# Kernel optimization log

Measured on AMD Instinct MI355X. Metric: run time of the kernel, lower is better.

The kernel has to match this reference:

```python
import jax, jax.numpy as jnp
import numpy as np

B, DIN, DOUT, NW = 32768, 768, 768, 48
NH = NW // 3  # num_haar == num_mexican == num_morlet == 16 for NW=48
OMEGA0 = 5.0
LN_EPS = 1e-5


def setup_inputs() -> dict:
    key = jax.random.key(0)
    ks = jax.random.split(key, 6)
    x = jax.random.normal(ks[0], (B, DIN), dtype=jnp.float32)
    # kaiming-normal-ish fan_in init for linear layers, zero bias
    W = jax.random.normal(ks[1], (DOUT, DIN), dtype=jnp.float32) / np.sqrt(DIN)
    b = jnp.zeros((DOUT,), jnp.float32)
    Wp = jax.random.normal(ks[2], (NW, DIN), dtype=jnp.float32) / np.sqrt(DIN)
    bp = jnp.zeros((NW,), jnp.float32)
    Wc = jax.random.normal(ks[3], (DOUT, NW), dtype=jnp.float32) / np.sqrt(NW)
    bc = jnp.zeros((DOUT,), jnp.float32)
    # mixed-type init: per-family logspace scales / linspace translations
    scales = jnp.asarray(np.concatenate([
        np.logspace(-0.5, 0.5, NH),
        np.logspace(-0.3, 0.7, NH),
        np.logspace(-0.3, 0.7, NW - 2 * NH)]), jnp.float32)
    translations = jnp.asarray(np.concatenate([
        np.linspace(-1.5, 1.5, NH),
        np.linspace(-1.5, 1.5, NH),
        np.linspace(-1.5, 1.5, NW - 2 * NH)]), jnp.float32)
    gamma = jnp.ones((DOUT,), jnp.float32)
    beta = jnp.zeros((DOUT,), jnp.float32)
    return {"x": x, "W": W, "b": b, "Wp": Wp, "bp": bp, "Wc": Wc,
            "bc": bc, "scales": scales, "translations": translations,
            "gamma": gamma, "beta": beta}


def _wavelet_basis(s):
    # s: [B, NW] already scaled/translated; columns split by family
    dt = s.dtype
    sh = s[:, :NH]
    haar = (((sh >= 0) & (sh < 0.5)).astype(dt)
            - ((sh >= 0.5) & (sh < 1.0)).astype(dt))
    sm = s[:, NH:2 * NH]
    mexican = (1.0 - sm * sm) * jnp.exp(-0.5 * sm * sm)
    so = s[:, 2 * NH:]
    morlet = jnp.cos(OMEGA0 * so) * jnp.exp(-0.5 * so * so)
    return jnp.concatenate([haar, mexican, morlet], axis=1)


def reference(x, W, b, Wp, bp, Wc, bc, scales, translations, gamma, beta):
    direct = x @ W.T + b                              # [B, DOUT]
    wi = x @ Wp.T + bp                                # [B, NW]
    s = (wi - translations) / scales                  # [B, NW]
    wav = jax.nn.gelu(_wavelet_basis(s), approximate=False)
    wpath = wav @ Wc.T + bc                           # [B, DOUT]
    h = direct + wpath
    mu = jnp.mean(h, axis=-1, keepdims=True)
    var = jnp.mean((h - mu) ** 2, axis=-1, keepdims=True)
    return (h - mu) * jax.lax.rsqrt(var + LN_EPS) * gamma + beta
```

## Files before the change

kernel.cpp:

```cpp
#include <hip/hip_runtime.h>
#include <math.h>


#define B_SZ  32768
#define DIN   768
#define DOUT  768
#define NWAV  48

#define WF_OFF   0
#define WPH_OFF  589824
#define WPL_OFF  638976
#define WCF_OFF  688128

typedef short bf16x8 __attribute__((ext_vector_type(8)));
typedef float f32x16 __attribute__((ext_vector_type(16)));

__device__ __forceinline__ float bf2f(short u) {
    union { unsigned int i; float f; } v;
    v.i = ((unsigned int)(unsigned short)u) << 16;
    return v.f;
}
__device__ __forceinline__ short f2bf(float f) {
    union { float f; unsigned int i; } v; v.f = f;
    unsigned int r = v.i + 0x7FFFu + ((v.i >> 16) & 1u);
    return (short)(r >> 16);
}

__global__ __launch_bounds__(256) void pack_kernel(
    const float* __restrict__ W, const float* __restrict__ Wp,
    const float* __restrict__ Wc, short* __restrict__ ws)
{
    const int gw = (blockIdx.x * 256 + threadIdx.x) >> 6;
    const int L  = threadIdx.x & 63;
    const int lm = L & 31, half = L >> 5;

    if (gw < 1152) {
        const int cb = gw / 48, kb = gw % 48;
        const int row = cb * 32 + lm;
        const int k = kb * 16 + half * 8;
        bf16x8 o;
#pragma unroll
        for (int j = 0; j < 8; j++) o[j] = f2bf(W[(size_t)row * DIN + k + j]);
        *reinterpret_cast<bf16x8*>(&ws[WF_OFF + (size_t)gw * 512 + L * 8]) = o;
    } else if (gw < 1248) {
        const int t = gw - 1152;
        const int ct = t / 48, kb = t % 48;
        const int j = ct * 32 + lm;
        const int k = kb * 16 + half * 8;
        bf16x8 h, l;
#pragma unroll
        for (int jj = 0; jj < 8; jj++) {
            float v = (j < NWAV) ? Wp[(size_t)j * DIN + k + jj] : 0.f;
            const short hh = f2bf(v);
            h[jj] = hh;
            l[jj] = f2bf(v - bf2f(hh));
        }
        *reinterpret_cast<bf16x8*>(&ws[WPH_OFF + (size_t)t * 512 + L * 8]) = h;
        *reinterpret_cast<bf16x8*>(&ws[WPL_OFF + (size_t)t * 512 + L * 8]) = l;
    } else if (gw < 1320) {
        const int t = gw - 1248;
        const int cb = t / 3, kb = t % 3;
        const int row = cb * 32 + lm;
        const int k = kb * 16 + half * 8;
        bf16x8 o;
#pragma unroll
        for (int jj = 0; jj < 8; jj++) o[jj] = f2bf(Wc[(size_t)row * NWAV + k + jj]);
        *reinterpret_cast<bf16x8*>(&ws[WCF_OFF + (size_t)t * 512 + L * 8]) = o;
    }
}

__global__ __launch_bounds__(512, 2) void fused_kernel(
    const float* __restrict__ x, const short* __restrict__ ws,
    const float* __restrict__ Wp,
    const float* __restrict__ bp, const float* __restrict__ sc,
    const float* __restrict__ tr,
    const float* __restrict__ bb, const float* __restrict__ bc,
    const float* __restrict__ gm, const float* __restrict__ bt,
    float* __restrict__ out)
{
    __shared__ __align__(16) short xh[2][64 * 72];
    __shared__ __align__(16) short xl[2][64 * 72];
    __shared__ float redS[64 * 8], redQ[64 * 8];
    __shared__ float muA[64], rsA[64];
    __shared__ unsigned flags[64];
    __shared__ double dred[8];

    const short* WF  = ws + WF_OFF;
    const short* WPH = ws + WPH_OFF;
    const short* WPL = ws + WPL_OFF;
    const short* WCF = ws + WCF_OFF;

    const int tid = threadIdx.x;
    const int r0  = blockIdx.x * 64;
    const int L   = tid & 63;
    const int wv  = __builtin_amdgcn_readfirstlane(tid >> 6);
    const int lm  = L & 31, half = L >> 5;
    const int L8  = L * 8;
    const bool wi = (wv < 4);
    const int wv3 = wv * 3;
    const int wrt = wv & 1, wct = wv >> 1;
    const int wct48 = wct * 48;

    if (tid < 64) flags[tid] = 0u;

    f32x16 acc[2][3];
#pragma unroll
    for (int rt = 0; rt < 2; rt++)
#pragma unroll
        for (int ct = 0; ct < 3; ct++)
#pragma unroll
            for (int g = 0; g < 16; g++) acc[rt][ct][g] = 0.f;
    f32x16 wacc;
#pragma unroll
    for (int g = 0; g < 16; g++) wacc[g] = 0.f;

    const int srow = tid >> 3;
    const int sk   = (tid & 7) * 8;

    {
        const float4* xp = reinterpret_cast<const float4*>(&x[(size_t)(r0 + srow) * DIN + sk]);
        const float4 v0 = xp[0], v1 = xp[1];
        const float f[8] = {v0.x, v0.y, v0.z, v0.w, v1.x, v1.y, v1.z, v1.w};
        bf16x8 hh, ll;
#pragma unroll
        for (int i = 0; i < 8; i++) {
            const short h = f2bf(f[i]);
            hh[i] = h;
            ll[i] = f2bf(f[i] - bf2f(h));
        }
        *reinterpret_cast<bf16x8*>(&xh[0][srow * 72 + sk]) = hh;
        *reinterpret_cast<bf16x8*>(&xl[0][srow * 72 + sk]) = ll;
    }
    __syncthreads();

    for (int k0i = 0; k0i < 12; ++k0i) {
        const int cur = k0i & 1;
        const int kb0 = k0i * 4;

        bf16x8 bfr[4][3];
#pragma unroll
        for (int ks = 0; ks < 4; ++ks)
#pragma unroll
            for (int ct = 0; ct < 3; ++ct)
                bfr[ks][ct] = *reinterpret_cast<const bf16x8*>(
                    &WF[((size_t)((wv3 + ct) * 48 + kb0 + ks)) * 512 + L8]);
        bf16x8 bwh[4], bwl[4];
        if (wi) {
#pragma unroll
            for (int ks = 0; ks < 4; ++ks) {
                bwh[ks] = *reinterpret_cast<const bf16x8*>(
                    &WPH[((size_t)(wct48 + kb0 + ks)) * 512 + L8]);
                bwl[ks] = *reinterpret_cast<const bf16x8*>(
                    &WPL[((size_t)(wct48 + kb0 + ks)) * 512 + L8]);
            }
        }

        float4 v0, v1;
        if (k0i < 11) {
            const float4* xp = reinterpret_cast<const float4*>(
                &x[(size_t)(r0 + srow) * DIN + (k0i + 1) * 64 + sk]);
            v0 = xp[0]; v1 = xp[1];
        }

        __builtin_amdgcn_sched_barrier(0);

#pragma unroll
        for (int ks = 0; ks < 4; ++ks) {
            const bf16x8 a0 = *reinterpret_cast<bf16x8*>(
                &xh[cur][lm * 72 + ks * 16 + half * 8]);
            const bf16x8 a1 = *reinterpret_cast<bf16x8*>(
                &xh[cur][(32 + lm) * 72 + ks * 16 + half * 8]);
#pragma unroll
            for (int ct = 0; ct < 3; ++ct) {
                acc[0][ct] = __builtin_amdgcn_mfma_f32_32x32x16_bf16(a0, bfr[ks][ct], acc[0][ct], 0, 0, 0);
                acc[1][ct] = __builtin_amdgcn_mfma_f32_32x32x16_bf16(a1, bfr[ks][ct], acc[1][ct], 0, 0, 0);
            }
            if (wi) {
                const bf16x8 ah = wrt ? a1 : a0;
                const bf16x8 al = *reinterpret_cast<bf16x8*>(
                    &xl[cur][(wrt * 32 + lm) * 72 + ks * 16 + half * 8]);
                wacc = __builtin_amdgcn_mfma_f32_32x32x16_bf16(ah, bwl[ks], wacc, 0, 0, 0);
                wacc = __builtin_amdgcn_mfma_f32_32x32x16_bf16(al, bwh[ks], wacc, 0, 0, 0);
                wacc = __builtin_amdgcn_mfma_f32_32x32x16_bf16(ah, bwh[ks], wacc, 0, 0, 0);
            }
        }

        if (k0i < 11) {
            const float f[8] = {v0.x, v0.y, v0.z, v0.w, v1.x, v1.y, v1.z, v1.w};
            bf16x8 hh, ll;
#pragma unroll
            for (int i = 0; i < 8; i++) {
                const short h = f2bf(f[i]);
                hh[i] = h;
                ll[i] = f2bf(f[i] - bf2f(h));
            }
            *reinterpret_cast<bf16x8*>(&xh[1 - cur][srow * 72 + sk]) = hh;
            *reinterpret_cast<bf16x8*>(&xl[1 - cur][srow * 72 + sk]) = ll;
        }
        __syncthreads();
    }

    short* wavL = &xh[0][0];
    if (wi) {
        const int j = wct * 32 + lm;
        if (j < NWAV) {
            const float bpv = bp[j], scv = sc[j], trv = tr[j];
#pragma unroll
            for (int g = 0; g < 16; ++g) {
                const int rowl = wrt * 32 + (g & 3) + 8 * (g >> 2) + 4 * half;
                const float wiv = wacc[g] + bpv;
                const float s = (wiv - trv) / scv;
                float w;
                if (j < 16) {
                    const float dmin = fminf(fabsf(s), fminf(fabsf(s - 0.5f), fabsf(s - 1.0f)));
                    if (dmin < 2e-4f) atomicOr(&flags[rowl], 1u << j);
                    w = (s >= 0.f && s < 0.5f) ? 1.f : ((s >= 0.5f && s < 1.f) ? -1.f : 0.f);
                } else if (j < 32) {
                    w = (1.f - s * s) * expf(-0.5f * s * s);
                } else {
                    w = cosf(5.f * s) * expf(-0.5f * s * s);
                }
                const float gel = 0.5f * w * (1.f + erff(w * 0.70710678118654752f));
                wavL[rowl * 72 + j] = f2bf(gel);
            }
        }
    }
    __syncthreads();

#pragma unroll 1
    for (int fr = 0; fr < 64; ++fr) {
        unsigned m = flags[fr];
        while (m) {
            const int j = __ffs(m) - 1;
            m &= m - 1;
            const float* xr = &x[(size_t)(r0 + fr) * DIN];
            const float* wr = &Wp[(size_t)j * DIN];
            double a = (double)xr[tid] * (double)wr[tid];
            if (tid < DIN - 512)
                a += (double)xr[tid + 512] * (double)wr[tid + 512];
            a += __shfl_xor(a, 1);  a += __shfl_xor(a, 2);
            a += __shfl_xor(a, 4);  a += __shfl_xor(a, 8);
            a += __shfl_xor(a, 16); a += __shfl_xor(a, 32);
            if (L == 0) dred[wv] = a;
            __syncthreads();
            if (tid == 0) {
                double wid = (double)bp[j];
#pragma unroll
                for (int i = 0; i < 8; i++) wid += dred[i];
                const double sd = (wid - (double)tr[j]) / (double)sc[j];
                const double w = (sd >= 0.0 && sd < 0.5) ? 1.0
                               : ((sd >= 0.5 && sd < 1.0) ? -1.0 : 0.0);
                const double gel = 0.5 * w * (1.0 + erf(w * 0.70710678118654752));
                wavL[fr * 72 + j] = f2bf((float)gel);
            }
            __syncthreads();
        }
    }

#pragma unroll
    for (int ks = 0; ks < 3; ++ks) {
        const bf16x8 a0 = *reinterpret_cast<bf16x8*>(&wavL[lm * 72 + ks * 16 + half * 8]);
        const bf16x8 a1 = *reinterpret_cast<bf16x8*>(&wavL[(32 + lm) * 72 + ks * 16 + half * 8]);
#pragma unroll
        for (int ct = 0; ct < 3; ++ct) {
            const bf16x8 b = *reinterpret_cast<const bf16x8*>(
                &WCF[((size_t)((wv3 + ct) * 3 + ks)) * 512 + L8]);
            acc[0][ct] = __builtin_amdgcn_mfma_f32_32x32x16_bf16(a0, b, acc[0][ct], 0, 0, 0);
            acc[1][ct] = __builtin_amdgcn_mfma_f32_32x32x16_bf16(a1, b, acc[1][ct], 0, 0, 0);
        }
    }

    float bias[3], gmv[3], btv[3];
#pragma unroll
    for (int ct = 0; ct < 3; ++ct) {
        const int col = wv * 96 + ct * 32 + lm;
        bias[ct] = bb[col] + bc[col];
        gmv[ct] = gm[col];
        btv[ct] = bt[col];
    }
#pragma unroll
    for (int rt = 0; rt < 2; ++rt) {
#pragma unroll
        for (int g = 0; g < 16; ++g) {
            const float v0 = acc[rt][0][g] + bias[0];
            const float v1 = acc[rt][1][g] + bias[1];
            const float v2 = acc[rt][2][g] + bias[2];
            acc[rt][0][g] = v0; acc[rt][1][g] = v1; acc[rt][2][g] = v2;
            float s1 = v0 + v1 + v2;
            float s2 = v0 * v0 + v1 * v1 + v2 * v2;
            s1 += __shfl_xor(s1, 1);  s2 += __shfl_xor(s2, 1);
            s1 += __shfl_xor(s1, 2);  s2 += __shfl_xor(s2, 2);
            s1 += __shfl_xor(s1, 4);  s2 += __shfl_xor(s2, 4);
            s1 += __shfl_xor(s1, 8);  s2 += __shfl_xor(s2, 8);
            s1 += __shfl_xor(s1, 16); s2 += __shfl_xor(s2, 16);
            if (lm == 0) {
                const int rowl = rt * 32 + (g & 3) + 8 * (g >> 2) + 4 * half;
                redS[rowl * 8 + wv] = s1;
                redQ[rowl * 8 + wv] = s2;
            }
        }
    }
    __syncthreads();
    if (tid < 64) {
        float S = 0.f, Q = 0.f;
#pragma unroll
        for (int i = 0; i < 8; i++) { S += redS[tid * 8 + i]; Q += redQ[tid * 8 + i]; }
        const float mu = S * (1.f / 768.f);
        const float var = Q * (1.f / 768.f) - mu * mu;
        muA[tid] = mu;
        rsA[tid] = rsqrtf(var + 1e-5f);
    }
    __syncthreads();

#pragma unroll
    for (int rt = 0; rt < 2; ++rt) {
#pragma unroll
        for (int g = 0; g < 16; ++g) {
            const int rowl = rt * 32 + (g & 3) + 8 * (g >> 2) + 4 * half;
            const float mu = muA[rowl], rs = rsA[rowl];
            float* orow = &out[(size_t)(r0 + rowl) * DOUT + wv * 96 + lm];
#pragma unroll
            for (int ct = 0; ct < 3; ++ct) {
                orow[ct * 32] = (acc[rt][ct][g] - mu) * rs * gmv[ct] + btv[ct];
            }
        }
    }
}

extern "C" void kernel_launch(void* const* d_in, const int* in_sizes, int n_in,
                              void* d_out, int out_size, void* d_ws, size_t ws_size,
                              hipStream_t stream)
{
    const float* x  = (const float*)d_in[0];
    const float* W  = (const float*)d_in[1];
    const float* b  = (const float*)d_in[2];
    const float* Wp = (const float*)d_in[3];
    const float* bp = (const float*)d_in[4];
    const float* Wc = (const float*)d_in[5];
    const float* bc = (const float*)d_in[6];
    const float* sc = (const float*)d_in[7];
    const float* tr = (const float*)d_in[8];
    const float* gm = (const float*)d_in[9];
    const float* bt = (const float*)d_in[10];
    float* out = (float*)d_out;
    short* ws  = (short*)d_ws;

    pack_kernel<<<dim3(330), dim3(256), 0, stream>>>(W, Wp, Wc, ws);
    fused_kernel<<<dim3(B_SZ / 64), dim3(512), 0, stream>>>(
        x, ws, Wp, bp, sc, tr, b, bc, gm, bt, out);
}
```

Measured before the change: 264.9 us.

## Merge weight packing into a persistent cooperative kernel with grid sync and float4 stores

```diff
diff --git a/kernel.cpp b/kernel.cpp
--- a/kernel.cpp
+++ b/kernel.cpp
@@ -1,5 +1,8 @@
 #include <hip/hip_runtime.h>
+#include <hip/hip_cooperative_groups.h>
 #include <math.h>
+
+namespace cg = cooperative_groups;
 
 
 #define B_SZ  32768
@@ -26,52 +29,10 @@
     return (short)(r >> 16);
 }
 
-__global__ __launch_bounds__(256) void pack_kernel(
-    const float* __restrict__ W, const float* __restrict__ Wp,
-    const float* __restrict__ Wc, short* __restrict__ ws)
-{
-    const int gw = (blockIdx.x * 256 + threadIdx.x) >> 6;
-    const int L  = threadIdx.x & 63;
-    const int lm = L & 31, half = L >> 5;
-
-    if (gw < 1152) {
-        const int cb = gw / 48, kb = gw % 48;
-        const int row = cb * 32 + lm;
-        const int k = kb * 16 + half * 8;
-        bf16x8 o;
-#pragma unroll
-        for (int j = 0; j < 8; j++) o[j] = f2bf(W[(size_t)row * DIN + k + j]);
-        *reinterpret_cast<bf16x8*>(&ws[WF_OFF + (size_t)gw * 512 + L * 8]) = o;
-    } else if (gw < 1248) {
-        const int t = gw - 1152;
-        const int ct = t / 48, kb = t % 48;
-        const int j = ct * 32 + lm;
-        const int k = kb * 16 + half * 8;
-        bf16x8 h, l;
-#pragma unroll
-        for (int jj = 0; jj < 8; jj++) {
-            float v = (j < NWAV) ? Wp[(size_t)j * DIN + k + jj] : 0.f;
-            const short hh = f2bf(v);
-            h[jj] = hh;
-            l[jj] = f2bf(v - bf2f(hh));
-        }
-        *reinterpret_cast<bf16x8*>(&ws[WPH_OFF + (size_t)t * 512 + L * 8]) = h;
-        *reinterpret_cast<bf16x8*>(&ws[WPL_OFF + (size_t)t * 512 + L * 8]) = l;
-    } else if (gw < 1320) {
-        const int t = gw - 1248;
-        const int cb = t / 3, kb = t % 3;
-        const int row = cb * 32 + lm;
-        const int k = kb * 16 + half * 8;
-        bf16x8 o;
-#pragma unroll
-        for (int jj = 0; jj < 8; jj++) o[jj] = f2bf(Wc[(size_t)row * NWAV + k + jj]);
-        *reinterpret_cast<bf16x8*>(&ws[WCF_OFF + (size_t)t * 512 + L * 8]) = o;
-    }
-}
-
 __global__ __launch_bounds__(512, 2) void fused_kernel(
-    const float* __restrict__ x, const short* __restrict__ ws,
-    const float* __restrict__ Wp,
+    const float* __restrict__ x,  const float* __restrict__ W,
+    const float* __restrict__ Wp, const float* __restrict__ Wc,
+    short* __restrict__ ws,
     const float* __restrict__ bp, const float* __restrict__ sc,
     const float* __restrict__ tr,
     const float* __restrict__ bb, const float* __restrict__ bc,
@@ -85,13 +46,7 @@
     __shared__ unsigned flags[64];
     __shared__ double dred[8];
 
-    const short* WF  = ws + WF_OFF;
-    const short* WPH = ws + WPH_OFF;
-    const short* WPL = ws + WPL_OFF;
-    const short* WCF = ws + WCF_OFF;
-
     const int tid = threadIdx.x;
-    const int r0  = blockIdx.x * 64;
     const int L   = tid & 63;
     const int wv  = __builtin_amdgcn_readfirstlane(tid >> 6);
     const int lm  = L & 31, half = L >> 5;
@@ -101,91 +56,74 @@
     const int wrt = wv & 1, wct = wv >> 1;
     const int wct48 = wct * 48;
 
-    if (tid < 64) flags[tid] = 0u;
-
-    f32x16 acc[2][3];
-#pragma unroll
-    for (int rt = 0; rt < 2; rt++)
-#pragma unroll
-        for (int ct = 0; ct < 3; ct++)
-#pragma unroll
-            for (int g = 0; g < 16; g++) acc[rt][ct][g] = 0.f;
-    f32x16 wacc;
-#pragma unroll
-    for (int g = 0; g < 16; g++) wacc[g] = 0.f;
+    {
+        const int gw = blockIdx.x * 8 + wv;
+        if (gw < 1152) {
+            const int cb = gw / 48, kb = gw % 48;
+            const int row = cb * 32 + lm;
+            const int k = kb * 16 + half * 8;
+            bf16x8 o;
+#pragma unroll
+            for (int j = 0; j < 8; j++) o[j] = f2bf(W[(size_t)row * DIN + k + j]);
+            *reinterpret_cast<bf16x8*>(&ws[WF_OFF + (size_t)gw * 512 + L8]) = o;
+        } else if (gw < 1248) {
+            const int t = gw - 1152;
+            const int ct = t / 48, kb = t % 48;
+            const int j = ct * 32 + lm;
+            const int k = kb * 16 + half * 8;
+            bf16x8 h, l;
+#pragma unroll
+            for (int jj = 0; jj < 8; jj++) {
+                float v = (j < NWAV) ? Wp[(size_t)j * DIN + k + jj] : 0.f;
+                const short hh = f2bf(v);
+                h[jj] = hh;
+                l[jj] = f2bf(v - bf2f(hh));
+            }
+            *reinterpret_cast<bf16x8*>(&ws[WPH_OFF + (size_t)t * 512 + L8]) = h;
+            *reinterpret_cast<bf16x8*>(&ws[WPL_OFF + (size_t)t * 512 + L8]) = l;
+        } else if (gw < 1320) {
+            const int t = gw - 1248;
+            const int cb = t / 3, kb = t % 3;
+            const int row = cb * 32 + lm;
+            const int k = kb * 16 + half * 8;
+            bf16x8 o;
+#pragma unroll
+            for (int jj = 0; jj < 8; jj++) o[jj] = f2bf(Wc[(size_t)row * NWAV + k + jj]);
+            *reinterpret_cast<bf16x8*>(&ws[WCF_OFF + (size_t)t * 512 + L8]) = o;
+        }
+    }
+    cg::this_grid().sync();
+
+    const short* WF  = ws + WF_OFF;
+    const short* WPH = ws + WPH_OFF;
+    const short* WPL = ws + WPL_OFF;
+    const short* WCF = ws + WCF_OFF;
 
     const int srow = tid >> 3;
     const int sk   = (tid & 7) * 8;
 
-    {
-        const float4* xp = reinterpret_cast<const float4*>(&x[(size_t)(r0 + srow) * DIN + sk]);
-        const float4 v0 = xp[0], v1 = xp[1];
-        const float f[8] = {v0.x, v0.y, v0.z, v0.w, v1.x, v1.y, v1.z, v1.w};
-        bf16x8 hh, ll;
-#pragma unroll
-        for (int i = 0; i < 8; i++) {
-            const short h = f2bf(f[i]);
-            hh[i] = h;
-            ll[i] = f2bf(f[i] - bf2f(h));
-        }
-        *reinterpret_cast<bf16x8*>(&xh[0][srow * 72 + sk]) = hh;
-        *reinterpret_cast<bf16x8*>(&xl[0][srow * 72 + sk]) = ll;
-    }
-    __syncthreads();
-
-    for (int k0i = 0; k0i < 12; ++k0i) {
-        const int cur = k0i & 1;
-        const int kb0 = k0i * 4;
-
-        bf16x8 bfr[4][3];
-#pragma unroll
-        for (int ks = 0; ks < 4; ++ks)
-#pragma unroll
-            for (int ct = 0; ct < 3; ++ct)
-                bfr[ks][ct] = *reinterpret_cast<const bf16x8*>(
-                    &WF[((size_t)((wv3 + ct) * 48 + kb0 + ks)) * 512 + L8]);
-        bf16x8 bwh[4], bwl[4];
-        if (wi) {
-#pragma unroll
-            for (int ks = 0; ks < 4; ++ks) {
-                bwh[ks] = *reinterpret_cast<const bf16x8*>(
-                    &WPH[((size_t)(wct48 + kb0 + ks)) * 512 + L8]);
-                bwl[ks] = *reinterpret_cast<const bf16x8*>(
-                    &WPL[((size_t)(wct48 + kb0 + ks)) * 512 + L8]);
-            }
-        }
-
-        float4 v0, v1;
-        if (k0i < 11) {
-            const float4* xp = reinterpret_cast<const float4*>(
-                &x[(size_t)(r0 + srow) * DIN + (k0i + 1) * 64 + sk]);
-            v0 = xp[0]; v1 = xp[1];
-        }
-
-        __builtin_amdgcn_sched_barrier(0);
-
-#pragma unroll
-        for (int ks = 0; ks < 4; ++ks) {
-            const bf16x8 a0 = *reinterpret_cast<bf16x8*>(
-                &xh[cur][lm * 72 + ks * 16 + half * 8]);
-            const bf16x8 a1 = *reinterpret_cast<bf16x8*>(
-                &xh[cur][(32 + lm) * 72 + ks * 16 + half * 8]);
-#pragma unroll
-            for (int ct = 0; ct < 3; ++ct) {
-                acc[0][ct] = __builtin_amdgcn_mfma_f32_32x32x16_bf16(a0, bfr[ks][ct], acc[0][ct], 0, 0, 0);
-                acc[1][ct] = __builtin_amdgcn_mfma_f32_32x32x16_bf16(a1, bfr[ks][ct], acc[1][ct], 0, 0, 0);
-            }
-            if (wi) {
-                const bf16x8 ah = wrt ? a1 : a0;
-                const bf16x8 al = *reinterpret_cast<bf16x8*>(
-                    &xl[cur][(wrt * 32 + lm) * 72 + ks * 16 + half * 8]);
-                wacc = __builtin_amdgcn_mfma_f32_32x32x16_bf16(ah, bwl[ks], wacc, 0, 0, 0);
-                wacc = __builtin_amdgcn_mfma_f32_32x32x16_bf16(al, bwh[ks], wacc, 0, 0, 0);
-                wacc = __builtin_amdgcn_mfma_f32_32x32x16_bf16(ah, bwh[ks], wacc, 0, 0, 0);
-            }
-        }
-
-        if (k0i < 11) {
+    const bool ib0 = (lm & 1) != 0, ib1 = (lm & 2) != 0;
+
+#pragma unroll 1
+    for (int pass = 0; pass < 2; ++pass) {
+        const int r0 = (blockIdx.x + (pass << 8)) * 64;
+
+        if (tid < 64) flags[tid] = 0u;
+
+        f32x16 acc[2][3];
+#pragma unroll
+        for (int rt = 0; rt < 2; rt++)
+#pragma unroll
+            for (int ct = 0; ct < 3; ct++)
+#pragma unroll
+                for (int g = 0; g < 16; g++) acc[rt][ct][g] = 0.f;
+        f32x16 wacc;
+#pragma unroll
+        for (int g = 0; g < 16; g++) wacc[g] = 0.f;
+
+        {
+            const float4* xp = reinterpret_cast<const float4*>(&x[(size_t)(r0 + srow) * DIN + sk]);
+            const float4 v0 = xp[0], v1 = xp[1];
             const float f[8] = {v0.x, v0.y, v0.z, v0.w, v1.x, v1.y, v1.z, v1.w};
             bf16x8 hh, ll;
 #pragma unroll
@@ -194,134 +132,231 @@
                 hh[i] = h;
                 ll[i] = f2bf(f[i] - bf2f(h));
             }
-            *reinterpret_cast<bf16x8*>(&xh[1 - cur][srow * 72 + sk]) = hh;
-            *reinterpret_cast<bf16x8*>(&xl[1 - cur][srow * 72 + sk]) = ll;
+            *reinterpret_cast<bf16x8*>(&xh[0][srow * 72 + sk]) = hh;
+            *reinterpret_cast<bf16x8*>(&xl[0][srow * 72 + sk]) = ll;
         }
         __syncthreads();
-    }
-
-    short* wavL = &xh[0][0];
-    if (wi) {
-        const int j = wct * 32 + lm;
-        if (j < NWAV) {
-            const float bpv = bp[j], scv = sc[j], trv = tr[j];
+
+        for (int k0i = 0; k0i < 12; ++k0i) {
+            const int cur = k0i & 1;
+            const int kb0 = k0i * 4;
+
+            bf16x8 bfr[4][3];
+#pragma unroll
+            for (int ks = 0; ks < 4; ++ks)
+#pragma unroll
+                for (int ct = 0; ct < 3; ++ct)
+                    bfr[ks][ct] = *reinterpret_cast<const bf16x8*>(
+                        &WF[((size_t)((wv3 + ct) * 48 + kb0 + ks)) * 512 + L8]);
+            bf16x8 bwh[4], bwl[4];
+            if (wi) {
+#pragma unroll
+                for (int ks = 0; ks < 4; ++ks) {
+                    bwh[ks] = *reinterpret_cast<const bf16x8*>(
+                        &WPH[((size_t)(wct48 + kb0 + ks)) * 512 + L8]);
+                    bwl[ks] = *reinterpret_cast<const bf16x8*>(
+                        &WPL[((size_t)(wct48 + kb0 + ks)) * 512 + L8]);
+                }
+            }
+
+            float4 v0, v1;
+            if (k0i < 11) {
+                const float4* xp = reinterpret_cast<const float4*>(
+                    &x[(size_t)(r0 + srow) * DIN + (k0i + 1) * 64 + sk]);
+                v0 = xp[0]; v1 = xp[1];
+            }
+
+            __builtin_amdgcn_sched_barrier(0);
+
+#pragma unroll
+            for (int ks = 0; ks < 4; ++ks) {
+                const bf16x8 a0 = *reinterpret_cast<bf16x8*>(
+                    &xh[cur][lm * 72 + ks * 16 + half * 8]);
+                const bf16x8 a1 = *reinterpret_cast<bf16x8*>(
+                    &xh[cur][(32 + lm) * 72 + ks * 16 + half * 8]);
+#pragma unroll
+                for (int ct = 0; ct < 3; ++ct) {
+                    acc[0][ct] = __builtin_amdgcn_mfma_f32_32x32x16_bf16(a0, bfr[ks][ct], acc[0][ct], 0, 0, 0);
+                    acc[1][ct] = __builtin_amdgcn_mfma_f32_32x32x16_bf16(a1, bfr[ks][ct], acc[1][ct], 0, 0, 0);
+                }
+                if (wi) {
+                    const bf16x8 ah = wrt ? a1 : a0;
+                    const bf16x8 al = *reinterpret_cast<bf16x8*>(
+                        &xl[cur][(wrt * 32 + lm) * 72 + ks * 16 + half * 8]);
+                    wacc = __builtin_amdgcn_mfma_f32_32x32x16_bf16(ah, bwl[ks], wacc, 0, 0, 0);
+                    wacc = __builtin_amdgcn_mfma_f32_32x32x16_bf16(al, bwh[ks], wacc, 0, 0, 0);
+                    wacc = __builtin_amdgcn_mfma_f32_32x32x16_bf16(ah, bwh[ks], wacc, 0, 0, 0);
+                }
+            }
+
+            if (k0i < 11) {
+                const float f[8] = {v0.x, v0.y, v0.z, v0.w, v1.x, v1.y, v1.z, v1.w};
+                bf16x8 hh, ll;
+#pragma unroll
+                for (int i = 0; i < 8; i++) {
+                    const short h = f2bf(f[i]);
+                    hh[i] = h;
+                    ll[i] = f2bf(f[i] - bf2f(h));
+                }
+                *reinterpret_cast<bf16x8*>(&xh[1 - cur][srow * 72 + sk]) = hh;
+                *reinterpret_cast<bf16x8*>(&xl[1 - cur][srow * 72 + sk]) = ll;
+            }
+            __syncthreads();
+        }
+
+        short* wavL = &xh[0][0];
+        if (wi) {
+            const int j = wct * 32 + lm;
+            if (j < NWAV) {
+                const float bpv = bp[j], scv = sc[j], trv = tr[j];
+#pragma unroll
+                for (int g = 0; g < 16; ++g) {
+                    const int rowl = wrt * 32 + (g & 3) + 8 * (g >> 2) + 4 * half;
+                    const float wiv = wacc[g] + bpv;
+                    const float s = (wiv - trv) / scv;
+                    float w;
+                    if (j < 16) {
+                        const float dmin = fminf(fabsf(s), fminf(fabsf(s - 0.5f), fabsf(s - 1.0f)));
+                        if (dmin < 2e-4f) atomicOr(&flags[rowl], 1u << j);
+                        w = (s >= 0.f && s < 0.5f) ? 1.f : ((s >= 0.5f && s < 1.f) ? -1.f : 0.f);
+                    } else if (j < 32) {
+                        w = (1.f - s * s) * expf(-0.5f * s * s);
+                    } else {
+                        w = cosf(5.f * s) * expf(-0.5f * s * s);
+                    }
+                    const float gel = 0.5f * w * (1.f + erff(w * 0.70710678118654752f));
+                    wavL[rowl * 72 + j] = f2bf(gel);
+                }
+            }
+        }
+        __syncthreads();
+
+#pragma unroll 1
+        for (int fr = 0; fr < 64; ++fr) {
+            unsigned m = flags[fr];
+            while (m) {
+                const int j = __ffs(m) - 1;
+                m &= m - 1;
+                const float* xr = &x[(size_t)(r0 + fr) * DIN];
+                const float* wr = &Wp[(size_t)j * DIN];
+                double a = (double)xr[tid] * (double)wr[tid];
+                if (tid < DIN - 512)
+                    a += (double)xr[tid + 512] * (double)wr[tid + 512];
+                a += __shfl_xor(a, 1);  a += __shfl_xor(a, 2);
+                a += __shfl_xor(a, 4);  a += __shfl_xor(a, 8);
+                a += __shfl_xor(a, 16); a += __shfl_xor(a, 32);
+                if (L == 0) dred[wv] = a;
+                __syncthreads();
+                if (tid == 0) {
+                    double wid = (double)bp[j];
+#pragma unroll
+                    for (int i = 0; i < 8; i++) wid += dred[i];
+                    const double sd = (wid - (double)tr[j]) / (double)sc[j];
+                    const double w = (sd >= 0.0 && sd < 0.5) ? 1.0
+                                   : ((sd >= 0.5 && sd < 1.0) ? -1.0 : 0.0);
+                    const double gel = 0.5 * w * (1.0 + erf(w * 0.70710678118654752));
+                    wavL[fr * 72 + j] = f2bf((float)gel);
+                }
+                __syncthreads();
+            }
+        }
+
+#pragma unroll
+        for (int ks = 0; ks < 3; ++ks) {
+            const bf16x8 a0 = *reinterpret_cast<bf16x8*>(&wavL[lm * 72 + ks * 16 + half * 8]);
+            const bf16x8 a1 = *reinterpret_cast<bf16x8*>(&wavL[(32 + lm) * 72 + ks * 16 + half * 8]);
+#pragma unroll
+            for (int ct = 0; ct < 3; ++ct) {
+                const bf16x8 b = *reinterpret_cast<const bf16x8*>(
+                    &WCF[((size_t)((wv3 + ct) * 3 + ks)) * 512 + L8]);
+                acc[0][ct] = __builtin_amdgcn_mfma_f32_32x32x16_bf16(a0, b, acc[0][ct], 0, 0, 0);
+                acc[1][ct] = __builtin_amdgcn_mfma_f32_32x32x16_bf16(a1, b, acc[1][ct], 0, 0, 0);
+            }
+        }
+
+        float bias[3];
+#pragma unroll
+        for (int ct = 0; ct < 3; ++ct) {
+            const int col = wv * 96 + ct * 32 + lm;
+            bias[ct] = bb[col] + bc[col];
+        }
+#pragma unroll
+        for (int rt = 0; rt < 2; ++rt) {
 #pragma unroll
             for (int g = 0; g < 16; ++g) {
-                const int rowl = wrt * 32 + (g & 3) + 8 * (g >> 2) + 4 * half;
-                const float wiv = wacc[g] + bpv;
-                const float s = (wiv - trv) / scv;
-                float w;
-                if (j < 16) {
-                    const float dmin = fminf(fabsf(s), fminf(fabsf(s - 0.5f), fabsf(s - 1.0f)));
-                    if (dmin < 2e-4f) atomicOr(&flags[rowl], 1u << j);
-                    w = (s >= 0.f && s < 0.5f) ? 1.f : ((s >= 0.5f && s < 1.f) ? -1.f : 0.f);
-                } else if (j < 32) {
-                    w = (1.f - s * s) * expf(-0.5f * s * s);
-                } else {
-                    w = cosf(5.f * s) * expf(-0.5f * s * s);
-                }
-                const float gel = 0.5f * w * (1.f + erff(w * 0.70710678118654752f));
-                wavL[rowl * 72 + j] = f2bf(gel);
-            }
-        }
-    }
-    __syncthreads();
-
-#pragma unroll 1
-    for (int fr = 0; fr < 64; ++fr) {
-        unsigned m = flags[fr];
-        while (m) {
-            const int j = __ffs(m) - 1;
-            m &= m - 1;
-            const float* xr = &x[(size_t)(r0 + fr) * DIN];
-            const float* wr = &Wp[(size_t)j * DIN];
-            double a = (double)xr[tid] * (double)wr[tid];
-            if (tid < DIN - 512)
-                a += (double)xr[tid + 512] * (double)wr[tid + 512];
-            a += __shfl_xor(a, 1);  a += __shfl_xor(a, 2);
-            a += __shfl_xor(a, 4);  a += __shfl_xor(a, 8);
-            a += __shfl_xor(a, 16); a += __shfl_xor(a, 32);
-            if (L == 0) dred[wv] = a;
-            __syncthreads();
-            if (tid == 0) {
-                double wid = (double)bp[j];
-#pragma unroll
-                for (int i = 0; i < 8; i++) wid += dred[i];
-                const double sd = (wid - (double)tr[j]) / (double)sc[j];
-                const double w = (sd >= 0.0 && sd < 0.5) ? 1.0
-                               : ((sd >= 0.5 && sd < 1.0) ? -1.0 : 0.0);
-                const double gel = 0.5 * w * (1.0 + erf(w * 0.70710678118654752));
-                wavL[fr * 72 + j] = f2bf((float)gel);
-            }
-            __syncthreads();
-        }
-    }
-
-#pragma unroll
-    for (int ks = 0; ks < 3; ++ks) {
-        const bf16x8 a0 = *reinterpret_cast<bf16x8*>(&wavL[lm * 72 + ks * 16 + half * 8]);
-        const bf16x8 a1 = *reinterpret_cast<bf16x8*>(&wavL[(32 + lm) * 72 + ks * 16 + half * 8]);
+                const float v0 = acc[rt][0][g] + bias[0];
+                const float v1 = acc[rt][1][g] + bias[1];
+                const float v2 = acc[rt][2][g] + bias[2];
+                acc[rt][0][g] = v0; acc[rt][1][g] = v1; acc[rt][2][g] = v2;
+                float s1 = v0 + v1 + v2;
+                float s2 = v0 * v0 + v1 * v1 + v2 * v2;
+                s1 += __shfl_xor(s1, 1);  s2 += __shfl_xor(s2, 1);
+                s1 += __shfl_xor(s1, 2);  s2 += __shfl_xor(s2, 2);
+                s1 += __shfl_xor(s1, 4);  s2 += __shfl_xor(s2, 4);
+                s1 += __shfl_xor(s1, 8);  s2 += __shfl_xor(s2, 8);
+                s1 += __shfl_xor(s1, 16); s2 += __shfl_xor(s2, 16);
+                if (lm == 0) {
+                    const int rowl = rt * 32 + (g & 3) + 8 * (g >> 2) + 4 * half;
+                    redS[rowl * 8 + wv] = s1;
+                    redQ[rowl * 8 + wv] = s2;
+                }
+            }
+        }
+        __syncthreads();
+        if (tid < 64) {
+            float S = 0.f, Q = 0.f;
+#pragma unroll
+            for (int i = 0; i < 8; i++) { S += redS[tid * 8 + i]; Q += redQ[tid * 8 + i]; }
+            const float mu = S * (1.f / 768.f);
+            const float var = Q * (1.f / 768.f) - mu * mu;
+            muA[tid] = mu;
+            rsA[tid] = rsqrtf(var + 1e-5f);
+        }
+        __syncthreads();
+
+        float4 g4[3], b4[3];
 #pragma unroll
         for (int ct = 0; ct < 3; ++ct) {
-            const bf16x8 b = *reinterpret_cast<const bf16x8*>(
-                &WCF[((size_t)((wv3 + ct) * 3 + ks)) * 512 + L8]);
-            acc[0][ct] = __builtin_amdgcn_mfma_f32_32x32x16_bf16(a0, b, acc[0][ct], 0, 0, 0);
-            acc[1][ct] = __builtin_amdgcn_mfma_f32_32x32x16_bf16(a1, b, acc[1][ct], 0, 0, 0);
-        }
-    }
-
-    float bias[3], gmv[3], btv[3];
-#pragma unroll
-    for (int ct = 0; ct < 3; ++ct) {
-        const int col = wv * 96 + ct * 32 + lm;
-        bias[ct] = bb[col] + bc[col];
-        gmv[ct] = gm[col];
-        btv[ct] = bt[col];
-    }
-#pragma unroll
-    for (int rt = 0; rt < 2; ++rt) {
-#pragma unroll
-        for (int g = 0; g < 16; ++g) {
-            const float v0 = acc[rt][0][g] + bias[0];
-            const float v1 = acc[rt][1][g] + bias[1];
-            const float v2 = acc[rt][2][g] + bias[2];
-            acc[rt][0][g] = v0; acc[rt][1][g] = v1; acc[rt][2][g] = v2;
-            float s1 = v0 + v1 + v2;
-            float s2 = v0 * v0 + v1 * v1 + v2 * v2;
-            s1 += __shfl_xor(s1, 1);  s2 += __shfl_xor(s2, 1);
-            s1 += __shfl_xor(s1, 2);  s2 += __shfl_xor(s2, 2);
-            s1 += __shfl_xor(s1, 4);  s2 += __shfl_xor(s2, 4);
-            s1 += __shfl_xor(s1, 8);  s2 += __shfl_xor(s2, 8);
-            s1 += __shfl_xor(s1, 16); s2 += __shfl_xor(s2, 16);
-            if (lm == 0) {
-                const int rowl = rt * 32 + (g & 3) + 8 * (g >> 2) + 4 * half;
-                redS[rowl * 8 + wv] = s1;
-                redQ[rowl * 8 + wv] = s2;
-            }
-        }
-    }
-    __syncthreads();
-    if (tid < 64) {
-        float S = 0.f, Q = 0.f;
-#pragma unroll
-        for (int i = 0; i < 8; i++) { S += redS[tid * 8 + i]; Q += redQ[tid * 8 + i]; }
-        const float mu = S * (1.f / 768.f);
-        const float var = Q * (1.f / 768.f) - mu * mu;
-        muA[tid] = mu;
-        rsA[tid] = rsqrtf(var + 1e-5f);
-    }
-    __syncthreads();
-
-#pragma unroll
-    for (int rt = 0; rt < 2; ++rt) {
-#pragma unroll
-        for (int g = 0; g < 16; ++g) {
-            const int rowl = rt * 32 + (g & 3) + 8 * (g >> 2) + 4 * half;
-            const float mu = muA[rowl], rs = rsA[rowl];
-            float* orow = &out[(size_t)(r0 + rowl) * DOUT + wv * 96 + lm];
-#pragma unroll
-            for (int ct = 0; ct < 3; ++ct) {
-                orow[ct * 32] = (acc[rt][ct][g] - mu) * rs * gmv[ct] + btv[ct];
+            const int colq = wv * 96 + ct * 32 + (lm & ~3);
+            g4[ct] = *reinterpret_cast<const float4*>(&gm[colq]);
+            b4[ct] = *reinterpret_cast<const float4*>(&bt[colq]);
+        }
+#pragma unroll
+        for (int rt = 0; rt < 2; ++rt) {
+#pragma unroll
+            for (int m = 0; m < 4; ++m) {
+                const int row = rt * 32 + 8 * m + 4 * half + (lm & 3);
+                const float mu = muA[row], rs = rsA[row];
+#pragma unroll
+                for (int ct = 0; ct < 3; ++ct) {
+                    const float v0 = acc[rt][ct][4 * m + 0];
+                    const float v1 = acc[rt][ct][4 * m + 1];
+                    const float v2 = acc[rt][ct][4 * m + 2];
+                    const float v3 = acc[rt][ct][4 * m + 3];
+                    const float t0 = __shfl_xor(v1, 1);
+                    const float t1 = __shfl_xor(v0, 1);
+                    const float t2 = __shfl_xor(v3, 1);
+                    const float t3 = __shfl_xor(v2, 1);
+                    const float b0 = ib0 ? t0 : v0;
+                    const float b1 = ib0 ? v1 : t1;
+                    const float b2 = ib0 ? t2 : v2;
+                    const float b3 = ib0 ? v3 : t3;
+                    const float u0 = __shfl_xor(b2, 2);
+                    const float u1 = __shfl_xor(b3, 2);
+                    const float u2 = __shfl_xor(b0, 2);
+                    const float u3 = __shfl_xor(b1, 2);
+                    const float c0 = ib1 ? u0 : b0;
+                    const float c1 = ib1 ? u1 : b1;
+                    const float c2 = ib1 ? b2 : u2;
+                    const float c3 = ib1 ? b3 : u3;
+                    float4 o;
+                    o.x = (c0 - mu) * rs * g4[ct].x + b4[ct].x;
+                    o.y = (c1 - mu) * rs * g4[ct].y + b4[ct].y;
+                    o.z = (c2 - mu) * rs * g4[ct].z + b4[ct].z;
+                    o.w = (c3 - mu) * rs * g4[ct].w + b4[ct].w;
+                    *reinterpret_cast<float4*>(
+                        &out[(size_t)(r0 + row) * DOUT + wv * 96 + ct * 32 + (lm & ~3)]) = o;
+                }
             }
         }
     }
@@ -345,7 +380,11 @@
     float* out = (float*)d_out;
     short* ws  = (short*)d_ws;
 
-    pack_kernel<<<dim3(330), dim3(256), 0, stream>>>(W, Wp, Wc, ws);
-    fused_kernel<<<dim3(B_SZ / 64), dim3(512), 0, stream>>>(
-        x, ws, Wp, bp, sc, tr, b, bc, gm, bt, out);
+    void* args[] = {
+        (void*)&x, (void*)&W, (void*)&Wp, (void*)&Wc, (void*)&ws,
+        (void*)&bp, (void*)&sc, (void*)&tr, (void*)&b, (void*)&bc,
+        (void*)&gm, (void*)&bt, (void*)&out
+    };
+    hipLaunchCooperativeKernel((void*)fused_kernel, dim3(256), dim3(512),
+                               args, 0, stream);
 }
```

Measured after the change: 468.7 us. +76.9%, slower.
